# Performance work log

Measured on AMD Instinct MI355X. Metric: run time of the kernel, lower is better.

## Reference

```python
import jax, jax.numpy as jnp
import numpy as np

DN = ('NCHW', 'OIHW', 'NCHW')

def conv2d(x, w, b):
    y = jax.lax.conv_general_dilated(x, w, (1, 1), 'SAME', dimension_numbers=DN)
    return y + b[None, :, None, None]

def deform_conv2d(x, offset, w, b):
    # torchvision DeformConv2d v1: kernel 3x3, stride 1, pad 1, dilation 1, no mask.
    # offset: [B, 18, H, W] ordered (dy0, dx0, dy1, dx1, ...) over row-major kernel taps.
    B, C, H, W = x.shape
    K2 = 9
    ki = (jnp.arange(K2) // 3).astype(x.dtype)  # kernel row index i
    kj = (jnp.arange(K2) % 3).astype(x.dtype)   # kernel col index j
    dy = offset[:, 0::2]  # [B, 9, H, W]
    dx = offset[:, 1::2]
    hh = jnp.arange(H, dtype=x.dtype)
    ww = jnp.arange(W, dtype=x.dtype)
    # sampling positions: p = out_pos - pad + k + offset
    py = hh[None, None, :, None] + ki[None, :, None, None] - 1.0 + dy  # [B,9,H,W]
    px = ww[None, None, None, :] + kj[None, :, None, None] - 1.0 + dx

    xf = x.reshape(B, C, H * W)
    y0 = jnp.floor(py); x0 = jnp.floor(px)
    y1 = y0 + 1.0;      x1 = x0 + 1.0
    wy1 = py - y0; wy0 = 1.0 - wy1
    wx1 = px - x0; wx0 = 1.0 - wx1

    def corner(yc, xc, cw):
        valid = (yc >= 0) & (yc <= H - 1) & (xc >= 0) & (xc <= W - 1)
        yi = jnp.clip(yc, 0, H - 1).astype(jnp.int32)
        xi = jnp.clip(xc, 0, W - 1).astype(jnp.int32)
        idx = yi * W + xi                       # [B,9,H,W]
        v = jax.vmap(lambda img, i: img[:, i])(xf, idx)  # [B,C,9,H,W]
        return v * (cw * valid.astype(x.dtype))[:, None]

    sampled = (corner(y0, x0, wy0 * wx0) + corner(y0, x1, wy0 * wx1)
               + corner(y1, x0, wy1 * wx0) + corner(y1, x1, wy1 * wx1))  # [B,C,9,H,W]
    out = jnp.einsum('bckhw,ock->bohw', sampled, w.reshape(w.shape[0], C, K2))
    return out + b[None, :, None, None]

def setup_inputs() -> dict:
    key = jax.random.key(0)
    ks = jax.random.split(key, 20)
    B, C, H, W = 8, 64, 128, 128
    O = 64
    s = 0.05
    inp = {
        'x': jax.random.normal(ks[0], (B, C, H, W), jnp.float32),
        'bsize': jax.random.uniform(ks[1], (B, 2), jnp.float32),
        # glob: Linear(2,64) -> ReLU -> Linear(64,32)
        'gw1': s * jax.random.normal(ks[2], (64, 2), jnp.float32),
        'gb1': jnp.zeros((64,), jnp.float32),
        'gw2': s * jax.random.normal(ks[3], (32, 64), jnp.float32),
        'gb2': jnp.zeros((32,), jnp.float32),
        # local: Conv2d(C,32,3) -> ReLU -> Conv2d(32,32,3)
        'lw1': s * jax.random.normal(ks[4], (32, C, 3, 3), jnp.float32),
        'lb1': jnp.zeros((32,), jnp.float32),
        'lw2': s * jax.random.normal(ks[5], (32, 32, 3, 3), jnp.float32),
        'lb2': jnp.zeros((32,), jnp.float32),
        # fuse: Conv2d(64,32,3) -> ReLU -> Conv2d(32,18,3)
        'fw1': s * jax.random.normal(ks[6], (32, 64, 3, 3), jnp.float32),
        'fb1': jnp.zeros((32,), jnp.float32),
        'fw2': s * jax.random.normal(ks[7], (18, 32, 3, 3), jnp.float32),
        'fb2': jnp.zeros((18,), jnp.float32),
        # deformable conv weight (copied from the source nn.Conv2d) + its own bias
        'dw': s * jax.random.normal(ks[8], (O, C, 3, 3), jnp.float32),
        'db': jnp.zeros((O,), jnp.float32),
    }
    return inp

def reference(x, bsize, gw1, gb1, gw2, gb2, lw1, lb1, lw2, lb2,
              fw1, fb1, fw2, fb2, dw, db):
    B, C, H, W = x.shape
    # global branch: MLP on box-size -> broadcast over spatial dims
    g = jax.nn.relu(bsize @ gw1.T + gb1) @ gw2.T + gb2          # [B,32]
    g_offset = jnp.broadcast_to(g[:, :, None, None], (B, 32, H, W))
    # local branch
    l_offset = conv2d(jax.nn.relu(conv2d(x, lw1, lb1)), lw2, lb2)  # [B,32,H,W]
    # fuse -> 18 offset channels
    fused = jnp.concatenate((g_offset, l_offset), axis=1)          # [B,64,H,W]
    offset = conv2d(jax.nn.relu(conv2d(fused, fw1, fb1)), fw2, fb2)  # [B,18,H,W]
    fea = deform_conv2d(x, offset, dw, db)
    return jax.nn.relu(fea)
```

## Files before the change

### kernel.cpp

```cpp
#include <hip/hip_runtime.h>

#define BB 8
#define CC 64
#define HH 128
#define WW 128
#define HWSZ (HH*WW)

typedef _Float16 h16;
typedef __attribute__((ext_vector_type(8))) _Float16 h16x8;
typedef __attribute__((ext_vector_type(4))) _Float16 h16x4;
typedef __attribute__((ext_vector_type(2))) _Float16 h16x2;
typedef __attribute__((ext_vector_type(4))) float f32x4;

__global__ __launch_bounds__(512) void g_mlp_kernel(
    const float* __restrict__ bsize, const float* __restrict__ gw1,
    const float* __restrict__ gb1, const float* __restrict__ gw2,
    const float* __restrict__ gb2, float* __restrict__ g) {
  __shared__ float h[BB][64];
  int t = threadIdx.x;
  if (t < BB * 64) {
    int b = t >> 6, i = t & 63;
    float v = fmaf(bsize[b * 2 + 0], gw1[i * 2 + 0],
                   fmaf(bsize[b * 2 + 1], gw1[i * 2 + 1], gb1[i]));
    h[b][i] = fmaxf(v, 0.f);
  }
  __syncthreads();
  if (t < BB * 32) {
    int b = t >> 5, j = t & 31;
    float acc = gb2[j];
#pragma unroll
    for (int i = 0; i < 64; ++i) acc = fmaf(h[b][i], gw2[j * 64 + i], acc);
    g[b * 32 + j] = acc;
  }
}

__device__ __forceinline__ void conv_pack(int j, int NCG, const float* w,
                                          int maxo, h16* dst) {
  int e = j & 7, l4 = (j >> 3) & 3, l15 = (j >> 5) & 15, f = (j >> 9) & 1;
  int cg = (j >> 10) & (NCG - 1), kt = (j >> 10) / NCG;
  int o = f * 16 + l15, c = cg * 32 + l4 * 8 + e;
  int CINw = NCG * 32;
  dst[j] = (o < maxo) ? (h16)w[(o * CINw + c) * 9 + kt] : (h16)0.f;
}

__global__ __launch_bounds__(256) void wprep_kernel(
    const float* __restrict__ lw1, const float* __restrict__ lw2,
    const float* __restrict__ fw1, const float* __restrict__ fw2,
    const float* __restrict__ dw, h16* __restrict__ cwq,
    h16* __restrict__ dwq) {
  int i = blockIdx.x * 256 + threadIdx.x;
  if (i < 18432) {
    conv_pack(i, 2, lw1, 32, cwq);
  } else if (i < 27648) {
    conv_pack(i - 18432, 1, lw2, 32, cwq + 18432);
  } else if (i < 46080) {
    conv_pack(i - 27648, 2, fw1, 32, cwq + 27648);
  } else if (i < 55296) {
    conv_pack(i - 46080, 1, fw2, 18, cwq + 46080);
  } else if (i < 55296 + 36864) {
    int j = i - 55296;
    int e = j & 7, l4 = (j >> 3) & 3, l15 = (j >> 5) & 15;
    int og = (j >> 9) & 3, cg = (j >> 11) & 1, kt = j >> 12;
    int o = og * 16 + l15, c = cg * 32 + l4 * 8 + e;
    dwq[j] = (h16)dw[(o * 64 + c) * 9 + kt];
  }
}

__global__ __launch_bounds__(256) void xtprep_kernel(
    const float* __restrict__ x, h16* __restrict__ xt) {
  int wg = (blockIdx.x & 7) * 64 + (blockIdx.x >> 3);
  int t = wg * 256 + threadIdx.x;
  int b = t >> 14, p = t & 16383;
  const float* xb = x + (size_t)b * 64 * HWSZ + p;
  h16* ob = xt + (size_t)t * 64;
#pragma unroll
  for (int c0 = 0; c0 < 64; c0 += 8) {
    h16x8 v;
#pragma unroll
    for (int i = 0; i < 8; ++i) v[i] = (h16)xb[(size_t)(c0 + i) * HWSZ];
    *(h16x8*)(ob + c0) = v;
  }
}

template <int NCG, bool GFUSE, bool RELU, int OMODE>
__global__ __launch_bounds__(256) void conv_mfma_kernel(
    const h16* __restrict__ in, const h16* __restrict__ cwq,
    const float* __restrict__ bias, const float* __restrict__ g,
    h16* __restrict__ outv) {
  constexpr int CINS = GFUSE ? 32 : NCG * 32;
  constexpr int NS = CINS / 8;
  constexpr int LOG2NS = (NS == 8) ? 3 : 2;
  __shared__ __align__(16) h16 sh[3 * 128 * CINS];
  const int wgid = (blockIdx.x & 7) * 128 + (blockIdx.x >> 3);
  const int b = wgid >> 7, h = wgid & 127;
  const int lane = threadIdx.x & 63, wave = threadIdx.x >> 6;
  const int l15 = lane & 15, l4 = lane >> 4;
  const h16* inb = in + (size_t)b * HWSZ * CINS;

  for (int q = threadIdx.x; q < 3 * 128 * NS; q += 256) {
    int s = q & (NS - 1), pr = q >> LOG2NS;
    int r = pr >> 7, px = pr & 127;
    int gy = min(max(h - 1 + r, 0), HH - 1);
    h16x8 v = *(const h16x8*)(inb + ((size_t)gy * WW + px) * CINS + s * 8);
    *(h16x8*)(sh + pr * CINS + ((s ^ (px & (NS - 1))) * 8)) = v;
  }

  const h16x8 zfr = {0, 0, 0, 0, 0, 0, 0, 0};
  h16x8 gfr = zfr;
  if (GFUSE) {
#pragma unroll
    for (int i = 0; i < 8; ++i) gfr[i] = (h16)g[b * 32 + l4 * 8 + i];
  }
  __syncthreads();

  f32x4 acc[2][2];
#pragma unroll
  for (int f = 0; f < 2; ++f)
#pragma unroll
    for (int j = 0; j < 2; ++j) acc[f][j] = (f32x4){0.f, 0.f, 0.f, 0.f};

#pragma unroll
  for (int kt = 0; kt < 9; ++kt) {
    const int ki = kt / 3 - 1, kj = kt % 3 - 1;
    const int y = h + ki;
    const bool yok = (unsigned)y < HH;
    const int r = ki + 1;
    int xs[2];
    bool ok[2];
#pragma unroll
    for (int j = 0; j < 2; ++j) {
      int xx = wave * 32 + j * 16 + l15 + kj;
      ok[j] = yok && ((unsigned)xx < WW);
      xs[j] = min(max(xx, 0), WW - 1);
    }
#pragma unroll
    for (int cg = 0; cg < NCG; ++cg) {
      const h16* aq = cwq + (size_t)((kt * NCG + cg) * 2) * 512 + l15 * 32 + l4 * 8;
      h16x8 afr0 = *(const h16x8*)(aq);
      h16x8 afr1 = *(const h16x8*)(aq + 512);
#pragma unroll
      for (int j = 0; j < 2; ++j) {
        h16x8 bv;
        if (GFUSE && cg == 0) {
          bv = ok[j] ? gfr : zfr;
        } else {
          const int s = (!GFUSE && NCG == 2) ? cg * 4 + l4 : l4;
          h16x8 ld = *(const h16x8*)(sh + (r * 128 + xs[j]) * CINS +
                                     ((s ^ (xs[j] & (NS - 1))) * 8));
          bv = ok[j] ? ld : zfr;
        }
        acc[0][j] = __builtin_amdgcn_mfma_f32_16x16x32_f16(afr0, bv, acc[0][j], 0, 0, 0);
        acc[1][j] = __builtin_amdgcn_mfma_f32_16x16x32_f16(afr1, bv, acc[1][j], 0, 0, 0);
      }
    }
  }
  if (OMODE == 0) {
    h16* ob = outv + (size_t)b * HWSZ * 32;
#pragma unroll
    for (int f = 0; f < 2; ++f)
#pragma unroll
      for (int j = 0; j < 2; ++j) {
        int p = h * WW + wave * 32 + j * 16 + l15;
        int o0 = f * 16 + l4 * 4;
        h16x4 st;
#pragma unroll
        for (int r2 = 0; r2 < 4; ++r2) {
          float v = acc[f][j][r2] + bias[o0 + r2];
          if (RELU) v = fmaxf(v, 0.f);
          st[r2] = (h16)v;
        }
        *(h16x4*)(ob + (size_t)p * 32 + o0) = st;
      }
  } else {
    h16* ob = outv + (size_t)b * HWSZ * 24;
#pragma unroll
    for (int j = 0; j < 2; ++j) {
      int p = h * WW + wave * 32 + j * 16 + l15;
      {
        int o0 = l4 * 4;
        h16x4 st;
#pragma unroll
        for (int r2 = 0; r2 < 4; ++r2) st[r2] = (h16)(acc[0][j][r2] + bias[o0 + r2]);
        *(h16x4*)(ob + (size_t)p * 24 + o0) = st;
      }
      if (l4 == 0) {
        h16x2 st2;
        st2[0] = (h16)(acc[1][j][0] + bias[16]);
        st2[1] = (h16)(acc[1][j][1] + bias[17]);
        *(h16x2*)(ob + (size_t)p * 24 + 16) = st2;
      }
    }
  }
}

__global__ __launch_bounds__(256) void deform_mfma_kernel(
    const h16* __restrict__ xt, const h16* __restrict__ offc,
    const h16* __restrict__ dwq, const float* __restrict__ db,
    float* __restrict__ out) {
  __shared__ __align__(16) h16 sh[5 * 72 * 64];
  const int wgid = (blockIdx.x & 7) * 256 + (blockIdx.x >> 3);
  const int b = wgid >> 8;
  const int rh = wgid & 255;
  const int h = rh >> 1;
  const int halfx = (rh & 1) * 64;
  const int x_lo = halfx - 4;
  const int lane = threadIdx.x & 63, wave = threadIdx.x >> 6;
  const int l15 = lane & 15, l4 = lane >> 4;
  const int wx = halfx + wave * 16;
  const int p0 = h * WW + wx;
  const int myw = wx + l15;
  const int mypix = p0 + l15;
  const h16* xb = xt + (size_t)b * HWSZ * 64;

#pragma unroll
  for (int it = 0; it < 12; ++it) {
    int q = it * 256 + threadIdx.x;
    if (q < 2880) {
      int s = q & 7, pr = q >> 3;
      int r = pr / 72, i = pr - r * 72;
      int gy = min(max(h - 2 + r, 0), HH - 1);
      int gx = min(max(x_lo + i, 0), WW - 1);
      h16x8 v = *(const h16x8*)(xb + ((size_t)gy * WW + gx) * 64 + s * 8);
      *(h16x8*)(sh + pr * 64 + ((s ^ (i & 7)) * 8)) = v;
    }
  }

  const h16* offp = offc + ((size_t)b * HWSZ + mypix) * 24;
  h16x8 offv0 = *(const h16x8*)(offp);
  h16x8 offv1 = *(const h16x8*)(offp + 8);
  h16x8 offv2 = *(const h16x8*)(offp + 16);
  __syncthreads();

#define OFFE(e) ((e) < 8 ? (float)offv0[(e) & 7] : (e) < 16 ? (float)offv1[(e) & 7] : (float)offv2[(e) & 7])

  f32x4 acc[4];
#pragma unroll
  for (int og = 0; og < 4; ++og) acc[og] = (f32x4){0.f, 0.f, 0.f, 0.f};

  h16x8 pc[2][2][4];
  h16x8 pw[2][8];
  h16   pg[2][4];

#define PREF(kt, par) do {                                                  \
    float py = (float)(h + (kt) / 3 - 1) + OFFE(2 * (kt));                  \
    float px = (float)(myw + (kt) % 3 - 1) + OFFE(2 * (kt) + 1);            \
    float y0f = floorf(py), x0f = floorf(px);                               \
    float wy1 = py - y0f, wy0 = 1.f - wy1;                                  \
    float wx1 = px - x0f, wx0 = 1.f - wx1;                                  \
    int y0 = (int)y0f, x0i = (int)x0f;                                      \
    int y1 = y0 + 1, x1i = x0i + 1;                                         \
    bool y0ok = (unsigned)y0 < HH, y1ok = (unsigned)y1 < HH;                \
    bool x0ok = (unsigned)x0i < WW, x1ok = (unsigned)x1i < WW;              \
    pg[par][0] = (h16)((y0ok && x0ok) ? wy0 * wx0 : 0.f);                   \
    pg[par][1] = (h16)((y0ok && x1ok) ? wy0 * wx1 : 0.f);                   \
    pg[par][2] = (h16)((y1ok && x0ok) ? wy1 * wx0 : 0.f);                   \
    pg[par][3] = (h16)((y1ok && x1ok) ? wy1 * wx1 : 0.f);                   \
    int y0c = min(max(y0, 0), HH - 1), y1c = min(max(y1, 0), HH - 1);       \
    int x0c = min(max(x0i, 0), WW - 1), x1c = min(max(x1i, 0), WW - 1);     \
    int ty0u = y0c - (h - 2), ty1u = y1c - (h - 2);                         \
    int tx0u = x0c - x_lo, tx1u = x1c - x_lo;                               \
    bool fast = ((unsigned)ty0u <= 4u) & ((unsigned)ty1u <= 4u) &           \
                ((unsigned)tx0u <= 71u) & ((unsigned)tx1u <= 71u);          \
    int ty0 = min(max(ty0u, 0), 4), ty1 = min(max(ty1u, 0), 4);             \
    int tx0 = min(max(tx0u, 0), 71), tx1 = min(max(tx1u, 0), 71);           \
    int pr00 = (ty0 * 72 + tx0) * 64, pr01 = (ty0 * 72 + tx1) * 64;         \
    int pr10 = (ty1 * 72 + tx0) * 64, pr11 = (ty1 * 72 + tx1) * 64;         \
    int sx0 = (tx0 & 7) * 8, sx1 = (tx1 & 7) * 8;                           \
    _Pragma("unroll")                                                       \
    for (int cg = 0; cg < 2; ++cg) {                                        \
      int sb = (cg * 4 + l4) * 8;                                           \
      pc[par][cg][0] = *(const h16x8*)(sh + pr00 + (sb ^ sx0));             \
      pc[par][cg][1] = *(const h16x8*)(sh + pr01 + (sb ^ sx1));             \
      pc[par][cg][2] = *(const h16x8*)(sh + pr10 + (sb ^ sx0));             \
      pc[par][cg][3] = *(const h16x8*)(sh + pr11 + (sb ^ sx1));             \
    }                                                                       \
    if (!fast) {                                                            \
      int i00 = y0c * WW + x0c, i01 = y0c * WW + x1c;                       \
      int i10 = y1c * WW + x0c, i11 = y1c * WW + x1c;                       \
      _Pragma("unroll")                                                     \
      for (int cg = 0; cg < 2; ++cg) {                                      \
        const h16* cb = xb + cg * 32 + l4 * 8;                              \
        pc[par][cg][0] = *(const h16x8*)(cb + (size_t)i00 * 64);            \
        pc[par][cg][1] = *(const h16x8*)(cb + (size_t)i01 * 64);            \
        pc[par][cg][2] = *(const h16x8*)(cb + (size_t)i10 * 64);            \
        pc[par][cg][3] = *(const h16x8*)(cb + (size_t)i11 * 64);            \
      }                                                                     \
    }                                                                       \
    const h16* wq0 = dwq + ((size_t)((kt) * 2 + 0) * 64 + l15) * 32 + l4 * 8; \
    const h16* wq1 = dwq + ((size_t)((kt) * 2 + 1) * 64 + l15) * 32 + l4 * 8; \
    pw[par][0] = *(const h16x8*)(wq0 + 0 * 512);                            \
    pw[par][1] = *(const h16x8*)(wq0 + 1 * 512);                            \
    pw[par][2] = *(const h16x8*)(wq0 + 2 * 512);                            \
    pw[par][3] = *(const h16x8*)(wq0 + 3 * 512);                            \
    pw[par][4] = *(const h16x8*)(wq1 + 0 * 512);                            \
    pw[par][5] = *(const h16x8*)(wq1 + 1 * 512);                            \
    pw[par][6] = *(const h16x8*)(wq1 + 2 * 512);                            \
    pw[par][7] = *(const h16x8*)(wq1 + 3 * 512);                            \
  } while (0)

#define CONS(par) do {                                                      \
    h16 w00 = pg[par][0], w01 = pg[par][1], w10 = pg[par][2], w11 = pg[par][3]; \
    h16x8 s0 = pc[par][0][0] * w00 + pc[par][0][1] * w01                    \
             + pc[par][0][2] * w10 + pc[par][0][3] * w11;                   \
    h16x8 s1 = pc[par][1][0] * w00 + pc[par][1][1] * w01                    \
             + pc[par][1][2] * w10 + pc[par][1][3] * w11;                   \
    acc[0] = __builtin_amdgcn_mfma_f32_16x16x32_f16(s0, pw[par][0], acc[0], 0, 0, 0); \
    acc[1] = __builtin_amdgcn_mfma_f32_16x16x32_f16(s0, pw[par][1], acc[1], 0, 0, 0); \
    acc[2] = __builtin_amdgcn_mfma_f32_16x16x32_f16(s0, pw[par][2], acc[2], 0, 0, 0); \
    acc[3] = __builtin_amdgcn_mfma_f32_16x16x32_f16(s0, pw[par][3], acc[3], 0, 0, 0); \
    acc[0] = __builtin_amdgcn_mfma_f32_16x16x32_f16(s1, pw[par][4], acc[0], 0, 0, 0); \
    acc[1] = __builtin_amdgcn_mfma_f32_16x16x32_f16(s1, pw[par][5], acc[1], 0, 0, 0); \
    acc[2] = __builtin_amdgcn_mfma_f32_16x16x32_f16(s1, pw[par][6], acc[2], 0, 0, 0); \
    acc[3] = __builtin_amdgcn_mfma_f32_16x16x32_f16(s1, pw[par][7], acc[3], 0, 0, 0); \
  } while (0)

  PREF(0, 0);
  PREF(1, 1);
  CONS(0);
  PREF(2, 0);
  CONS(1);
  PREF(3, 1);
  CONS(0);
  PREF(4, 0);
  CONS(1);
  PREF(5, 1);
  CONS(0);
  PREF(6, 0);
  CONS(1);
  PREF(7, 1);
  CONS(0);
  PREF(8, 0);
  CONS(1);
  CONS(0);
#undef PREF
#undef CONS
#undef OFFE

  float* outb = out + (size_t)b * CC * HWSZ;
#pragma unroll
  for (int og = 0; og < 4; ++og) {
    int o = og * 16 + l15;
    float bv = db[o];
    f32x4 st;
#pragma unroll
    for (int r = 0; r < 4; ++r) st[r] = fmaxf(acc[og][r] + bv, 0.f);
    *(f32x4*)(outb + (size_t)o * HWSZ + p0 + l4 * 4) = st;
  }
}

extern "C" void kernel_launch(void* const* d_in, const int* in_sizes, int n_in,
                              void* d_out, int out_size, void* d_ws, size_t ws_size,
                              hipStream_t stream) {
  const float* x     = (const float*)d_in[0];
  const float* bsize = (const float*)d_in[1];
  const float* gw1   = (const float*)d_in[2];
  const float* gb1   = (const float*)d_in[3];
  const float* gw2   = (const float*)d_in[4];
  const float* gb2   = (const float*)d_in[5];
  const float* lw1   = (const float*)d_in[6];
  const float* lb1   = (const float*)d_in[7];
  const float* lw2   = (const float*)d_in[8];
  const float* lb2   = (const float*)d_in[9];
  const float* fw1   = (const float*)d_in[10];
  const float* fb1   = (const float*)d_in[11];
  const float* fw2   = (const float*)d_in[12];
  const float* fb2   = (const float*)d_in[13];
  const float* dw    = (const float*)d_in[14];
  const float* db    = (const float*)d_in[15];
  float* out = (float*)d_out;

  float* gbuf = (float*)d_ws;
  h16* xt   = (h16*)((char*)d_ws + 2048);
  h16* offc = (h16*)((char*)d_ws + 2048 + (size_t)BB * HWSZ * 64 * 2);
  h16* dwq  = (h16*)((char*)offc + (size_t)BB * HWSZ * 24 * 2);

  h16* loff = (h16*)d_out;
  h16* cwq  = (h16*)d_out + 4194304;
  h16* t12  = (h16*)d_out + 8388608;
  const h16* lw1q = cwq;
  const h16* lw2q = cwq + 18432;
  const h16* fw1q = cwq + 27648;
  const h16* fw2q = cwq + 46080;

  g_mlp_kernel<<<1, 512, 0, stream>>>(bsize, gw1, gb1, gw2, gb2, gbuf);
  wprep_kernel<<<360, 256, 0, stream>>>(lw1, lw2, fw1, fw2, dw, cwq, dwq);
  xtprep_kernel<<<512, 256, 0, stream>>>(x, xt);
  conv_mfma_kernel<2, false, true, 0><<<1024, 256, 0, stream>>>(
      xt, lw1q, lb1, nullptr, t12);
  conv_mfma_kernel<1, false, false, 0><<<1024, 256, 0, stream>>>(
      t12, lw2q, lb2, nullptr, loff);
  conv_mfma_kernel<2, true, true, 0><<<1024, 256, 0, stream>>>(
      loff, fw1q, fb1, gbuf, t12);
  conv_mfma_kernel<1, false, false, 1><<<1024, 256, 0, stream>>>(
      t12, fw2q, fb2, nullptr, offc);
  deform_mfma_kernel<<<2048, 256, 0, stream>>>(xt, offc, dwq, db, out);
}
```

Measured before the change: 117.2 us.

## Split channel staging into two LDS phases in first conv and deform kernels

The first 3x3 conv (64 input channels) and the deformable conv now stage their input tile in shared memory in two 32-channel halves, with a barrier between phases, instead of staging all 64 channels at once. This halves LDS usage per workgroup and, in the deform kernel, halves the prefetch register arrays, which is meant to allow more resident workgroups and better latency hiding. In exchange it adds extra barriers and serialises staging with compute, and the deform kernel recomputes sampling coordinates and bilinear weights for each channel half.

New measurement: 148.7 us. 26.8% more time.

```diff
diff --git a/kernel.cpp b/kernel.cpp
--- a/kernel.cpp
+++ b/kernel.cpp
@@ -82,28 +82,21 @@
   }
 }
 
-template <int NCG, bool GFUSE, bool RELU, int OMODE>
+template <int NCG, bool GFUSE, bool RELU, int OMODE, int NPH>
 __global__ __launch_bounds__(256) void conv_mfma_kernel(
     const h16* __restrict__ in, const h16* __restrict__ cwq,
     const float* __restrict__ bias, const float* __restrict__ g,
     h16* __restrict__ outv) {
-  constexpr int CINS = GFUSE ? 32 : NCG * 32;
-  constexpr int NS = CINS / 8;
+  constexpr int ISTR = GFUSE ? 32 : NCG * 32;
+  constexpr int CSTG = (NPH == 2) ? ISTR / 2 : ISTR;
+  constexpr int NS = CSTG / 8;
   constexpr int LOG2NS = (NS == 8) ? 3 : 2;
-  __shared__ __align__(16) h16 sh[3 * 128 * CINS];
+  __shared__ __align__(16) h16 sh[3 * 128 * CSTG];
   const int wgid = (blockIdx.x & 7) * 128 + (blockIdx.x >> 3);
   const int b = wgid >> 7, h = wgid & 127;
   const int lane = threadIdx.x & 63, wave = threadIdx.x >> 6;
   const int l15 = lane & 15, l4 = lane >> 4;
-  const h16* inb = in + (size_t)b * HWSZ * CINS;
-
-  for (int q = threadIdx.x; q < 3 * 128 * NS; q += 256) {
-    int s = q & (NS - 1), pr = q >> LOG2NS;
-    int r = pr >> 7, px = pr & 127;
-    int gy = min(max(h - 1 + r, 0), HH - 1);
-    h16x8 v = *(const h16x8*)(inb + ((size_t)gy * WW + px) * CINS + s * 8);
-    *(h16x8*)(sh + pr * CINS + ((s ^ (px & (NS - 1))) * 8)) = v;
-  }
+  const h16* inb = in + (size_t)b * HWSZ * ISTR;
 
   const h16x8 zfr = {0, 0, 0, 0, 0, 0, 0, 0};
   h16x8 gfr = zfr;
@@ -111,7 +104,6 @@
 #pragma unroll
     for (int i = 0; i < 8; ++i) gfr[i] = (h16)g[b * 32 + l4 * 8 + i];
   }
-  __syncthreads();
 
   f32x4 acc[2][2];
 #pragma unroll
@@ -120,47 +112,62 @@
     for (int j = 0; j < 2; ++j) acc[f][j] = (f32x4){0.f, 0.f, 0.f, 0.f};
 
 #pragma unroll
-  for (int kt = 0; kt < 9; ++kt) {
-    const int ki = kt / 3 - 1, kj = kt % 3 - 1;
-    const int y = h + ki;
-    const bool yok = (unsigned)y < HH;
-    const int r = ki + 1;
-    int xs[2];
-    bool ok[2];
-#pragma unroll
-    for (int j = 0; j < 2; ++j) {
-      int xx = wave * 32 + j * 16 + l15 + kj;
-      ok[j] = yok && ((unsigned)xx < WW);
-      xs[j] = min(max(xx, 0), WW - 1);
+  for (int p = 0; p < NPH; ++p) {
+    if (p > 0) __syncthreads();
+    for (int q = threadIdx.x; q < 3 * 128 * NS; q += 256) {
+      int s = q & (NS - 1), pr = q >> LOG2NS;
+      int r = pr >> 7, px = pr & 127;
+      int gy = min(max(h - 1 + r, 0), HH - 1);
+      h16x8 v = *(const h16x8*)(inb + ((size_t)gy * WW + px) * ISTR + p * CSTG + s * 8);
+      *(h16x8*)(sh + pr * CSTG + ((s ^ (px & (NS - 1))) * 8)) = v;
     }
-#pragma unroll
-    for (int cg = 0; cg < NCG; ++cg) {
-      const h16* aq = cwq + (size_t)((kt * NCG + cg) * 2) * 512 + l15 * 32 + l4 * 8;
-      h16x8 afr0 = *(const h16x8*)(aq);
-      h16x8 afr1 = *(const h16x8*)(aq + 512);
+    __syncthreads();
+
+#pragma unroll
+    for (int kt = 0; kt < 9; ++kt) {
+      const int ki = kt / 3 - 1, kj = kt % 3 - 1;
+      const int y = h + ki;
+      const bool yok = (unsigned)y < HH;
+      const int r = ki + 1;
+      int xs[2];
+      bool ok[2];
 #pragma unroll
       for (int j = 0; j < 2; ++j) {
-        h16x8 bv;
-        if (GFUSE && cg == 0) {
-          bv = ok[j] ? gfr : zfr;
-        } else {
-          const int s = (!GFUSE && NCG == 2) ? cg * 4 + l4 : l4;
-          h16x8 ld = *(const h16x8*)(sh + (r * 128 + xs[j]) * CINS +
-                                     ((s ^ (xs[j] & (NS - 1))) * 8));
-          bv = ok[j] ? ld : zfr;
+        int xx = wave * 32 + j * 16 + l15 + kj;
+        ok[j] = yok && ((unsigned)xx < WW);
+        xs[j] = min(max(xx, 0), WW - 1);
+      }
+      const int cgLo = (NPH == 2) ? p : 0;
+      const int cgHi = (NPH == 2) ? p + 1 : NCG;
+#pragma unroll
+      for (int cg = cgLo; cg < cgHi; ++cg) {
+        const h16* aq = cwq + (size_t)((kt * NCG + cg) * 2) * 512 + l15 * 32 + l4 * 8;
+        h16x8 afr0 = *(const h16x8*)(aq);
+        h16x8 afr1 = *(const h16x8*)(aq + 512);
+#pragma unroll
+        for (int j = 0; j < 2; ++j) {
+          h16x8 bv;
+          if (GFUSE && cg == 0) {
+            bv = ok[j] ? gfr : zfr;
+          } else {
+            h16x8 ld = *(const h16x8*)(sh + (r * 128 + xs[j]) * CSTG +
+                                       ((l4 ^ (xs[j] & (NS - 1))) * 8));
+            bv = ok[j] ? ld : zfr;
+          }
+          acc[0][j] = __builtin_amdgcn_mfma_f32_16x16x32_f16(afr0, bv, acc[0][j], 0, 0, 0);
+          acc[1][j] = __builtin_amdgcn_mfma_f32_16x16x32_f16(afr1, bv, acc[1][j], 0, 0, 0);
         }
-        acc[0][j] = __builtin_amdgcn_mfma_f32_16x16x32_f16(afr0, bv, acc[0][j], 0, 0, 0);
-        acc[1][j] = __builtin_amdgcn_mfma_f32_16x16x32_f16(afr1, bv, acc[1][j], 0, 0, 0);
       }
     }
   }
+
   if (OMODE == 0) {
     h16* ob = outv + (size_t)b * HWSZ * 32;
 #pragma unroll
     for (int f = 0; f < 2; ++f)
 #pragma unroll
       for (int j = 0; j < 2; ++j) {
-        int p = h * WW + wave * 32 + j * 16 + l15;
+        int p2 = h * WW + wave * 32 + j * 16 + l15;
         int o0 = f * 16 + l4 * 4;
         h16x4 st;
 #pragma unroll
@@ -169,25 +176,25 @@
           if (RELU) v = fmaxf(v, 0.f);
           st[r2] = (h16)v;
         }
-        *(h16x4*)(ob + (size_t)p * 32 + o0) = st;
+        *(h16x4*)(ob + (size_t)p2 * 32 + o0) = st;
       }
   } else {
     h16* ob = outv + (size_t)b * HWSZ * 24;
 #pragma unroll
     for (int j = 0; j < 2; ++j) {
-      int p = h * WW + wave * 32 + j * 16 + l15;
+      int p2 = h * WW + wave * 32 + j * 16 + l15;
       {
         int o0 = l4 * 4;
         h16x4 st;
 #pragma unroll
         for (int r2 = 0; r2 < 4; ++r2) st[r2] = (h16)(acc[0][j][r2] + bias[o0 + r2]);
-        *(h16x4*)(ob + (size_t)p * 24 + o0) = st;
+        *(h16x4*)(ob + (size_t)p2 * 24 + o0) = st;
       }
       if (l4 == 0) {
         h16x2 st2;
         st2[0] = (h16)(acc[1][j][0] + bias[16]);
         st2[1] = (h16)(acc[1][j][1] + bias[17]);
-        *(h16x2*)(ob + (size_t)p * 24 + 16) = st2;
+        *(h16x2*)(ob + (size_t)p2 * 24 + 16) = st2;
       }
     }
   }
@@ -197,7 +204,7 @@
     const h16* __restrict__ xt, const h16* __restrict__ offc,
     const h16* __restrict__ dwq, const float* __restrict__ db,
     float* __restrict__ out) {
-  __shared__ __align__(16) h16 sh[5 * 72 * 64];
+  __shared__ __align__(16) h16 sh[5 * 72 * 32];
   const int wgid = (blockIdx.x & 7) * 256 + (blockIdx.x >> 3);
   const int b = wgid >> 8;
   const int rh = wgid & 255;
@@ -212,24 +219,26 @@
   const int mypix = p0 + l15;
   const h16* xb = xt + (size_t)b * HWSZ * 64;
 
-#pragma unroll
-  for (int it = 0; it < 12; ++it) {
-    int q = it * 256 + threadIdx.x;
-    if (q < 2880) {
-      int s = q & 7, pr = q >> 3;
-      int r = pr / 72, i = pr - r * 72;
-      int gy = min(max(h - 2 + r, 0), HH - 1);
-      int gx = min(max(x_lo + i, 0), WW - 1);
-      h16x8 v = *(const h16x8*)(xb + ((size_t)gy * WW + gx) * 64 + s * 8);
-      *(h16x8*)(sh + pr * 64 + ((s ^ (i & 7)) * 8)) = v;
-    }
-  }
-
+#define STAGE(cg) do {                                                      \
+    _Pragma("unroll")                                                       \
+    for (int it = 0; it < 6; ++it) {                                        \
+      int q = it * 256 + threadIdx.x;                                       \
+      if (q < 1440) {                                                       \
+        int s = q & 3, pr = q >> 2;                                         \
+        int r = pr / 72, i = pr - r * 72;                                   \
+        int gy = min(max(h - 2 + r, 0), HH - 1);                            \
+        int gx = min(max(x_lo + i, 0), WW - 1);                             \
+        h16x8 v = *(const h16x8*)(xb + ((size_t)gy * WW + gx) * 64 + (cg) * 32 + s * 8); \
+        *(h16x8*)(sh + pr * 32 + ((s ^ (i & 3)) * 8)) = v;                  \
+      }                                                                     \
+    }                                                                       \
+  } while (0)
+
+  STAGE(0);
   const h16* offp = offc + ((size_t)b * HWSZ + mypix) * 24;
   h16x8 offv0 = *(const h16x8*)(offp);
   h16x8 offv1 = *(const h16x8*)(offp + 8);
   h16x8 offv2 = *(const h16x8*)(offp + 16);
-  __syncthreads();
 
 #define OFFE(e) ((e) < 8 ? (float)offv0[(e) & 7] : (e) < 16 ? (float)offv1[(e) & 7] : (float)offv2[(e) & 7])
 
@@ -237,11 +246,11 @@
 #pragma unroll
   for (int og = 0; og < 4; ++og) acc[og] = (f32x4){0.f, 0.f, 0.f, 0.f};
 
-  h16x8 pc[2][2][4];
-  h16x8 pw[2][8];
+  h16x8 pc[2][4];
+  h16x8 pw[2][4];
   h16   pg[2][4];
 
-#define PREF(kt, par) do {                                                  \
+#define PREF(kt, par, cg) do {                                              \
     float py = (float)(h + (kt) / 3 - 1) + OFFE(2 * (kt));                  \
     float px = (float)(myw + (kt) % 3 - 1) + OFFE(2 * (kt) + 1);            \
     float y0f = floorf(py), x0f = floorf(px);                               \
@@ -263,77 +272,58 @@
                 ((unsigned)tx0u <= 71u) & ((unsigned)tx1u <= 71u);          \
     int ty0 = min(max(ty0u, 0), 4), ty1 = min(max(ty1u, 0), 4);             \
     int tx0 = min(max(tx0u, 0), 71), tx1 = min(max(tx1u, 0), 71);           \
-    int pr00 = (ty0 * 72 + tx0) * 64, pr01 = (ty0 * 72 + tx1) * 64;         \
-    int pr10 = (ty1 * 72 + tx0) * 64, pr11 = (ty1 * 72 + tx1) * 64;         \
-    int sx0 = (tx0 & 7) * 8, sx1 = (tx1 & 7) * 8;                           \
-    _Pragma("unroll")                                                       \
-    for (int cg = 0; cg < 2; ++cg) {                                        \
-      int sb = (cg * 4 + l4) * 8;                                           \
-      pc[par][cg][0] = *(const h16x8*)(sh + pr00 + (sb ^ sx0));             \
-      pc[par][cg][1] = *(const h16x8*)(sh + pr01 + (sb ^ sx1));             \
-      pc[par][cg][2] = *(const h16x8*)(sh + pr10 + (sb ^ sx0));             \
-      pc[par][cg][3] = *(const h16x8*)(sh + pr11 + (sb ^ sx1));             \
-    }                                                                       \
+    int pr00 = (ty0 * 72 + tx0) * 32, pr01 = (ty0 * 72 + tx1) * 32;         \
+    int pr10 = (ty1 * 72 + tx0) * 32, pr11 = (ty1 * 72 + tx1) * 32;        \
+    int sx0 = (tx0 & 3) * 8, sx1 = (tx1 & 3) * 8;                           \
+    int sb = l4 * 8;                                                        \
+    pc[par][0] = *(const h16x8*)(sh + pr00 + (sb ^ sx0));                   \
+    pc[par][1] = *(const h16x8*)(sh + pr01 + (sb ^ sx1));                   \
+    pc[par][2] = *(const h16x8*)(sh + pr10 + (sb ^ sx0));                   \
+    pc[par][3] = *(const h16x8*)(sh + pr11 + (sb ^ sx1));                   \
     if (!fast) {                                                            \
       int i00 = y0c * WW + x0c, i01 = y0c * WW + x1c;                       \
       int i10 = y1c * WW + x0c, i11 = y1c * WW + x1c;                       \
-      _Pragma("unroll")                                                     \
-      for (int cg = 0; cg < 2; ++cg) {                                      \
-        const h16* cb = xb + cg * 32 + l4 * 8;                              \
-        pc[par][cg][0] = *(const h16x8*)(cb + (size_t)i00 * 64);            \
-        pc[par][cg][1] = *(const h16x8*)(cb + (size_t)i01 * 64);            \
-        pc[par][cg][2] = *(const h16x8*)(cb + (size_t)i10 * 64);            \
-        pc[par][cg][3] = *(const h16x8*)(cb + (size_t)i11 * 64);            \
-      }                                                                     \
+      const h16* cb = xb + (cg) * 32 + l4 * 8;                              \
+      pc[par][0] = *(const h16x8*)(cb + (size_t)i00 * 64);                  \
+      pc[par][1] = *(const h16x8*)(cb + (size_t)i01 * 64);                  \
+      pc[par][2] = *(const h16x8*)(cb + (size_t)i10 * 64);                  \
+      pc[par][3] = *(const h16x8*)(cb + (size_t)i11 * 64);                  \
     }                                                                       \
-    const h16* wq0 = dwq + ((size_t)((kt) * 2 + 0) * 64 + l15) * 32 + l4 * 8; \
-    const h16* wq1 = dwq + ((size_t)((kt) * 2 + 1) * 64 + l15) * 32 + l4 * 8; \
-    pw[par][0] = *(const h16x8*)(wq0 + 0 * 512);                            \
-    pw[par][1] = *(const h16x8*)(wq0 + 1 * 512);                            \
-    pw[par][2] = *(const h16x8*)(wq0 + 2 * 512);                            \
-    pw[par][3] = *(const h16x8*)(wq0 + 3 * 512);                            \
-    pw[par][4] = *(const h16x8*)(wq1 + 0 * 512);                            \
-    pw[par][5] = *(const h16x8*)(wq1 + 1 * 512);                            \
-    pw[par][6] = *(const h16x8*)(wq1 + 2 * 512);                            \
-    pw[par][7] = *(const h16x8*)(wq1 + 3 * 512);                            \
+    const h16* wq = dwq + ((size_t)((kt) * 2 + (cg)) * 64 + l15) * 32 + l4 * 8; \
+    pw[par][0] = *(const h16x8*)(wq + 0 * 512);                             \
+    pw[par][1] = *(const h16x8*)(wq + 1 * 512);                             \
+    pw[par][2] = *(const h16x8*)(wq + 2 * 512);                             \
+    pw[par][3] = *(const h16x8*)(wq + 3 * 512);                             \
   } while (0)
 
 #define CONS(par) do {                                                      \
-    h16 w00 = pg[par][0], w01 = pg[par][1], w10 = pg[par][2], w11 = pg[par][3]; \
-    h16x8 s0 = pc[par][0][0] * w00 + pc[par][0][1] * w01                    \
-             + pc[par][0][2] * w10 + pc[par][0][3] * w11;                   \
-    h16x8 s1 = pc[par][1][0] * w00 + pc[par][1][1] * w01                    \
-             + pc[par][1][2] * w10 + pc[par][1][3] * w11;                   \
-    acc[0] = __builtin_amdgcn_mfma_f32_16x16x32_f16(s0, pw[par][0], acc[0], 0, 0, 0); \
-    acc[1] = __builtin_amdgcn_mfma_f32_16x16x32_f16(s0, pw[par][1], acc[1], 0, 0, 0); \
-    acc[2] = __builtin_amdgcn_mfma_f32_16x16x32_f16(s0, pw[par][2], acc[2], 0, 0, 0); \
-    acc[3] = __builtin_amdgcn_mfma_f32_16x16x32_f16(s0, pw[par][3], acc[3], 0, 0, 0); \
-    acc[0] = __builtin_amdgcn_mfma_f32_16x16x32_f16(s1, pw[par][4], acc[0], 0, 0, 0); \
-    acc[1] = __builtin_amdgcn_mfma_f32_16x16x32_f16(s1, pw[par][5], acc[1], 0, 0, 0); \
-    acc[2] = __builtin_amdgcn_mfma_f32_16x16x32_f16(s1, pw[par][6], acc[2], 0, 0, 0); \
-    acc[3] = __builtin_amdgcn_mfma_f32_16x16x32_f16(s1, pw[par][7], acc[3], 0, 0, 0); \
+    h16x8 sv = pc[par][0] * pg[par][0] + pc[par][1] * pg[par][1]            \
+             + pc[par][2] * pg[par][2] + pc[par][3] * pg[par][3];           \
+    acc[0] = __builtin_amdgcn_mfma_f32_16x16x32_f16(sv, pw[par][0], acc[0], 0, 0, 0); \
+    acc[1] = __builtin_amdgcn_mfma_f32_16x16x32_f16(sv, pw[par][1], acc[1], 0, 0, 0); \
+    acc[2] = __builtin_amdgcn_mfma_f32_16x16x32_f16(sv, pw[par][2], acc[2], 0, 0, 0); \
+    acc[3] = __builtin_amdgcn_mfma_f32_16x16x32_f16(sv, pw[par][3], acc[3], 0, 0, 0); \
   } while (0)
 
-  PREF(0, 0);
-  PREF(1, 1);
-  CONS(0);
-  PREF(2, 0);
-  CONS(1);
-  PREF(3, 1);
-  CONS(0);
-  PREF(4, 0);
-  CONS(1);
-  PREF(5, 1);
-  CONS(0);
-  PREF(6, 0);
-  CONS(1);
-  PREF(7, 1);
-  CONS(0);
-  PREF(8, 0);
-  CONS(1);
-  CONS(0);
+#define PHASE(cg) do {                                                      \
+    PREF(0, 0, cg); PREF(1, 1, cg); CONS(0);                                \
+    PREF(2, 0, cg); CONS(1); PREF(3, 1, cg); CONS(0);                       \
+    PREF(4, 0, cg); CONS(1); PREF(5, 1, cg); CONS(0);                       \
+    PREF(6, 0, cg); CONS(1); PREF(7, 1, cg); CONS(0);                       \
+    PREF(8, 0, cg); CONS(1); CONS(0);                                       \
+  } while (0)
+
+  __syncthreads();
+  PHASE(0);
+  __syncthreads();
+  STAGE(1);
+  __syncthreads();
+  PHASE(1);
+
+#undef PHASE
 #undef PREF
 #undef CONS
+#undef STAGE
 #undef OFFE
 
   float* outb = out + (size_t)b * CC * HWSZ;
@@ -385,13 +375,13 @@
   g_mlp_kernel<<<1, 512, 0, stream>>>(bsize, gw1, gb1, gw2, gb2, gbuf);
   wprep_kernel<<<360, 256, 0, stream>>>(lw1, lw2, fw1, fw2, dw, cwq, dwq);
   xtprep_kernel<<<512, 256, 0, stream>>>(x, xt);
-  conv_mfma_kernel<2, false, true, 0><<<1024, 256, 0, stream>>>(
+  conv_mfma_kernel<2, false, true, 0, 2><<<1024, 256, 0, stream>>>(
       xt, lw1q, lb1, nullptr, t12);
-  conv_mfma_kernel<1, false, false, 0><<<1024, 256, 0, stream>>>(
+  conv_mfma_kernel<1, false, false, 0, 1><<<1024, 256, 0, stream>>>(
       t12, lw2q, lb2, nullptr, loff);
-  conv_mfma_kernel<2, true, true, 0><<<1024, 256, 0, stream>>>(
+  conv_mfma_kernel<2, true, true, 0, 1><<<1024, 256, 0, stream>>>(
       loff, fw1q, fb1, gbuf, t12);
-  conv_mfma_kernel<1, false, false, 1><<<1024, 256, 0, stream>>>(
+  conv_mfma_kernel<1, false, false, 1, 1><<<1024, 256, 0, stream>>>(
       t12, fw2q, fb2, nullptr, offc);
   deform_mfma_kernel<<<2048, 256, 0, stream>>>(xt, offc, dwq, db, out);
 }
```

## Merge prep kernels into one launch and stage deform output through LDS

Applied to the files above, without the earlier changes.

Combines the global MLP, weight packing and NCHW-to-NHWC fp16 transpose into a single prep kernel, with block ranges dispatching to each task. This removes two kernel launches and their gaps. Separately, the deform kernel's epilogue now writes results to shared memory and reads them back so each wave stores contiguous 256-byte rows per output channel, aiming for more coalesced global writes. The cost is two extra barriers and an LDS round trip. It also assumes the reused shared buffer is large enough and that halfx is defined in the unseen code.

New measurement: 111.0 us. 1.06x faster.

```diff
diff --git a/kernel.cpp b/kernel.cpp
--- a/kernel.cpp
+++ b/kernel.cpp
@@ -11,28 +11,6 @@
 typedef __attribute__((ext_vector_type(4))) _Float16 h16x4;
 typedef __attribute__((ext_vector_type(2))) _Float16 h16x2;
 typedef __attribute__((ext_vector_type(4))) float f32x4;
-
-__global__ __launch_bounds__(512) void g_mlp_kernel(
-    const float* __restrict__ bsize, const float* __restrict__ gw1,
-    const float* __restrict__ gb1, const float* __restrict__ gw2,
-    const float* __restrict__ gb2, float* __restrict__ g) {
-  __shared__ float h[BB][64];
-  int t = threadIdx.x;
-  if (t < BB * 64) {
-    int b = t >> 6, i = t & 63;
-    float v = fmaf(bsize[b * 2 + 0], gw1[i * 2 + 0],
-                   fmaf(bsize[b * 2 + 1], gw1[i * 2 + 1], gb1[i]));
-    h[b][i] = fmaxf(v, 0.f);
-  }
-  __syncthreads();
-  if (t < BB * 32) {
-    int b = t >> 5, j = t & 31;
-    float acc = gb2[j];
-#pragma unroll
-    for (int i = 0; i < 64; ++i) acc = fmaf(h[b][i], gw2[j * 64 + i], acc);
-    g[b * 32 + j] = acc;
-  }
-}
 
 __device__ __forceinline__ void conv_pack(int j, int NCG, const float* w,
                                           int maxo, h16* dst) {
@@ -43,42 +21,65 @@
   dst[j] = (o < maxo) ? (h16)w[(o * CINw + c) * 9 + kt] : (h16)0.f;
 }
 
-__global__ __launch_bounds__(256) void wprep_kernel(
+__global__ __launch_bounds__(256) void prep_kernel(
+    const float* __restrict__ bsize, const float* __restrict__ gw1,
+    const float* __restrict__ gb1, const float* __restrict__ gw2,
+    const float* __restrict__ gb2, float* __restrict__ g,
     const float* __restrict__ lw1, const float* __restrict__ lw2,
     const float* __restrict__ fw1, const float* __restrict__ fw2,
     const float* __restrict__ dw, h16* __restrict__ cwq,
-    h16* __restrict__ dwq) {
-  int i = blockIdx.x * 256 + threadIdx.x;
-  if (i < 18432) {
-    conv_pack(i, 2, lw1, 32, cwq);
-  } else if (i < 27648) {
-    conv_pack(i - 18432, 1, lw2, 32, cwq + 18432);
-  } else if (i < 46080) {
-    conv_pack(i - 27648, 2, fw1, 32, cwq + 27648);
-  } else if (i < 55296) {
-    conv_pack(i - 46080, 1, fw2, 18, cwq + 46080);
-  } else if (i < 55296 + 36864) {
-    int j = i - 55296;
-    int e = j & 7, l4 = (j >> 3) & 3, l15 = (j >> 5) & 15;
-    int og = (j >> 9) & 3, cg = (j >> 11) & 1, kt = j >> 12;
-    int o = og * 16 + l15, c = cg * 32 + l4 * 8 + e;
-    dwq[j] = (h16)dw[(o * 64 + c) * 9 + kt];
-  }
-}
-
-__global__ __launch_bounds__(256) void xtprep_kernel(
-    const float* __restrict__ x, h16* __restrict__ xt) {
-  int wg = (blockIdx.x & 7) * 64 + (blockIdx.x >> 3);
-  int t = wg * 256 + threadIdx.x;
-  int b = t >> 14, p = t & 16383;
-  const float* xb = x + (size_t)b * 64 * HWSZ + p;
-  h16* ob = xt + (size_t)t * 64;
-#pragma unroll
-  for (int c0 = 0; c0 < 64; c0 += 8) {
-    h16x8 v;
-#pragma unroll
-    for (int i = 0; i < 8; ++i) v[i] = (h16)xb[(size_t)(c0 + i) * HWSZ];
-    *(h16x8*)(ob + c0) = v;
+    h16* __restrict__ dwq, const float* __restrict__ x,
+    h16* __restrict__ xt) {
+  __shared__ float hbuf[BB][64];
+  const int blk = blockIdx.x;
+  const int tid = threadIdx.x;
+  if (blk == 0) {
+#pragma unroll
+    for (int i2 = 0; i2 < 2; ++i2) {
+      int idx = i2 * 256 + tid;
+      int b = idx >> 6, i = idx & 63;
+      float v = fmaf(bsize[b * 2 + 0], gw1[i * 2 + 0],
+                     fmaf(bsize[b * 2 + 1], gw1[i * 2 + 1], gb1[i]));
+      hbuf[b][i] = fmaxf(v, 0.f);
+    }
+    __syncthreads();
+    int b = tid >> 5, j = tid & 31;
+    float acc = gb2[j];
+#pragma unroll
+    for (int i = 0; i < 64; ++i) acc = fmaf(hbuf[b][i], gw2[j * 64 + i], acc);
+    g[b * 32 + j] = acc;
+  } else if (blk <= 360) {
+    int i = (blk - 1) * 256 + tid;
+    if (i < 18432) {
+      conv_pack(i, 2, lw1, 32, cwq);
+    } else if (i < 27648) {
+      conv_pack(i - 18432, 1, lw2, 32, cwq + 18432);
+    } else if (i < 46080) {
+      conv_pack(i - 27648, 2, fw1, 32, cwq + 27648);
+    } else if (i < 55296) {
+      conv_pack(i - 46080, 1, fw2, 18, cwq + 46080);
+    } else if (i < 55296 + 36864) {
+      int j = i - 55296;
+      int e = j & 7, l4 = (j >> 3) & 3, l15 = (j >> 5) & 15;
+      int og = (j >> 9) & 3, cg = (j >> 11) & 1, kt = j >> 12;
+      int o = og * 16 + l15, c = cg * 32 + l4 * 8 + e;
+      dwq[j] = (h16)dw[(o * 64 + c) * 9 + kt];
+    }
+  } else {
+    int j = blk - 361;
+    int b = (1 + j) & 7;
+    int slot = j >> 3;
+    int t = b * 16384 + slot * 256 + tid;
+    int p = t & 16383;
+    const float* xb = x + (size_t)b * 64 * HWSZ + p;
+    h16* ob = xt + (size_t)t * 64;
+#pragma unroll
+    for (int c0 = 0; c0 < 64; c0 += 8) {
+      h16x8 v;
+#pragma unroll
+      for (int i = 0; i < 8; ++i) v[i] = (h16)xb[(size_t)(c0 + i) * HWSZ];
+      *(h16x8*)(ob + c0) = v;
+    }
   }
 }
 
@@ -336,7 +337,8 @@
 #undef CONS
 #undef OFFE
 
-  float* outb = out + (size_t)b * CC * HWSZ;
+  __syncthreads();
+  float* shf = (float*)sh;
 #pragma unroll
   for (int og = 0; og < 4; ++og) {
     int o = og * 16 + l15;
@@ -344,7 +346,16 @@
     f32x4 st;
 #pragma unroll
     for (int r = 0; r < 4; ++r) st[r] = fmaxf(acc[og][r] + bv, 0.f);
-    *(f32x4*)(outb + (size_t)o * HWSZ + p0 + l4 * 4) = st;
+    *(f32x4*)(shf + o * 68 + wave * 16 + l4 * 4) = st;
+  }
+  __syncthreads();
+  float* outb = out + (size_t)b * CC * HWSZ + h * WW + halfx;
+#pragma unroll
+  for (int it2 = 0; it2 < 4; ++it2) {
+    int o = wave * 16 + it2 * 4 + (lane >> 4);
+    int px4 = (lane & 15) * 4;
+    f32x4 v = *(const f32x4*)(shf + o * 68 + px4);
+    *(f32x4*)(outb + (size_t)o * HWSZ + px4) = v;
   }
 }
 
@@ -382,9 +393,8 @@
   const h16* fw1q = cwq + 27648;
   const h16* fw2q = cwq + 46080;
 
-  g_mlp_kernel<<<1, 512, 0, stream>>>(bsize, gw1, gb1, gw2, gb2, gbuf);
-  wprep_kernel<<<360, 256, 0, stream>>>(lw1, lw2, fw1, fw2, dw, cwq, dwq);
-  xtprep_kernel<<<512, 256, 0, stream>>>(x, xt);
+  prep_kernel<<<873, 256, 0, stream>>>(bsize, gw1, gb1, gw2, gb2, gbuf,
+                                       lw1, lw2, fw1, fw2, dw, cwq, dwq, x, xt);
   conv_mfma_kernel<2, false, true, 0><<<1024, 256, 0, stream>>>(
       xt, lw1q, lb1, nullptr, t12);
   conv_mfma_kernel<1, false, false, 0><<<1024, 256, 0, stream>>>(
```
